# Performance work log

Measured on AMD Instinct MI355X. Metric: run time of the kernel, lower is better.

The kernel has to match this reference:

```python
import jax, jax.numpy as jnp
import numpy as np

POOL = 7          # pool_size
NUM_ROIS = 512    # num_rois
H, W, C = 64, 64, 1024


def setup_inputs() -> dict:
    key = jax.random.key(0)
    k1, k2, k3 = jax.random.split(key, 3)
    img = jax.random.normal(k1, (1, H, W, C), dtype=jnp.float32)
    # rois[0, i] = (x, y, w, h); guarantee x+w <= W and y+h <= H
    xy = jax.random.randint(k2, (1, NUM_ROIS, 2), 0, 32, dtype=jnp.int32)
    wh = jax.random.randint(k3, (1, NUM_ROIS, 2), 8, 33, dtype=jnp.int32)
    rois = jnp.concatenate([xy, wh], axis=-1)
    return {"img": img, "rois": rois}


def _roi_pool_one(img0, roi):
    # img0: [H, W, C]; roi: (x, y, w, h) int32
    # Faithful to tf.image.resize_images(bilinear, align_corners=False, TF1
    # legacy): src = dst * (in_size / out_size), corners clamped to the crop.
    x, y, w, h = roi[0], roi[1], roi[2], roi[3]
    i = jnp.arange(POOL, dtype=jnp.float32)
    sy = i * (h.astype(jnp.float32) / POOL)   # source row within crop
    sx = i * (w.astype(jnp.float32) / POOL)   # source col within crop
    y0 = jnp.floor(sy).astype(jnp.int32)       # always <= h-1 since sy < h
    x0 = jnp.floor(sx).astype(jnp.int32)
    fy = sy - y0.astype(jnp.float32)
    fx = sx - x0.astype(jnp.float32)
    y1 = jnp.minimum(y0 + 1, h - 1)            # clamp to crop edge
    x1 = jnp.minimum(x0 + 1, w - 1)
    gy0, gy1 = y + y0, y + y1                  # global feature-map indices
    gx0, gx1 = x + x0, x + x1
    # gather 4 bilinear corners: each [POOL, POOL, C]
    v00 = img0[gy0[:, None], gx0[None, :]]
    v01 = img0[gy0[:, None], gx1[None, :]]
    v10 = img0[gy1[:, None], gx0[None, :]]
    v11 = img0[gy1[:, None], gx1[None, :]]
    top = v00 + (v01 - v00) * fx[None, :, None]
    bot = v10 + (v11 - v10) * fx[None, :, None]
    return top + (bot - top) * fy[:, None, None]


def reference(img, rois):
    # vmap over ROIs replaces the Python-level per-ROI crop/resize loop
    out = jax.vmap(lambda r: _roi_pool_one(img[0], r))(rois[0])  # [R,P,P,C]
    return out[None]  # [1, num_rois, pool, pool, C]
```

## Files before the change

### kernel.cpp

```cpp
#include <hip/hip_runtime.h>

#define POOL 7
#define NUM_ROIS 512
#define IMG_H 64
#define IMG_W 64
#define IMG_C 1024

__global__ __launch_bounds__(256) void roi_pool_kernel(
    const float* __restrict__ img,
    const int*   __restrict__ rois,
    float*       __restrict__ out)
{
    const int b  = blockIdx.x;
    const int r  = b / 49;
    const int ij = b - r * 49;
    const int i  = ij / 7;
    const int j  = ij - i * 7;

    const int4 roi = reinterpret_cast<const int4*>(rois)[r];
    const int x = roi.x, y = roi.y, w = roi.z, h = roi.w;

    const float sy = (float)i * ((float)h / 7.0f);
    const float sx = (float)j * ((float)w / 7.0f);
    const int y0 = (int)floorf(sy);
    const int x0 = (int)floorf(sx);
    const float fy = sy - (float)y0;
    const float fx = sx - (float)x0;
    const int y1 = min(y0 + 1, h - 1);
    const int x1 = min(x0 + 1, w - 1);
    const int gy0 = y + y0, gy1 = y + y1;
    const int gx0 = x + x0, gx1 = x + x1;

    const int c = threadIdx.x * 4;

    const float4 v00 = *reinterpret_cast<const float4*>(&img[((size_t)gy0 * IMG_W + gx0) * IMG_C + c]);
    const float4 v01 = *reinterpret_cast<const float4*>(&img[((size_t)gy0 * IMG_W + gx1) * IMG_C + c]);
    const float4 v10 = *reinterpret_cast<const float4*>(&img[((size_t)gy1 * IMG_W + gx0) * IMG_C + c]);
    const float4 v11 = *reinterpret_cast<const float4*>(&img[((size_t)gy1 * IMG_W + gx1) * IMG_C + c]);

    float4 res;
    {
        const float t0 = v00.x + (v01.x - v00.x) * fx;
        const float b0 = v10.x + (v11.x - v10.x) * fx;
        res.x = t0 + (b0 - t0) * fy;
    }
    {
        const float t0 = v00.y + (v01.y - v00.y) * fx;
        const float b0 = v10.y + (v11.y - v10.y) * fx;
        res.y = t0 + (b0 - t0) * fy;
    }
    {
        const float t0 = v00.z + (v01.z - v00.z) * fx;
        const float b0 = v10.z + (v11.z - v10.z) * fx;
        res.z = t0 + (b0 - t0) * fy;
    }
    {
        const float t0 = v00.w + (v01.w - v00.w) * fx;
        const float b0 = v10.w + (v11.w - v10.w) * fx;
        res.w = t0 + (b0 - t0) * fy;
    }

    reinterpret_cast<float4*>(out)[(size_t)b * (IMG_C / 4) + threadIdx.x] = res;
}

extern "C" void kernel_launch(void* const* d_in, const int* in_sizes, int n_in,
                              void* d_out, int out_size, void* d_ws, size_t ws_size,
                              hipStream_t stream) {
    const float* img  = (const float*)d_in[0];
    const int*   rois = (const int*)d_in[1];
    float*       out  = (float*)d_out;

    const int grid = NUM_ROIS * POOL * POOL;
    roi_pool_kernel<<<grid, 256, 0, stream>>>(img, rois, out);
}
```

Measured before the change: 143.3 us.

## Process a full pooled row per block with XCD remap and nontemporal stores

```diff
diff --git a/kernel.cpp b/kernel.cpp
--- a/kernel.cpp
+++ b/kernel.cpp
@@ -2,65 +2,67 @@
 
 #define POOL 7
 #define NUM_ROIS 512
-#define IMG_H 64
 #define IMG_W 64
 #define IMG_C 1024
+#define NXCD 8
+
+typedef float vfloat4 __attribute__((ext_vector_type(4)));
 
 __global__ __launch_bounds__(256) void roi_pool_kernel(
     const float* __restrict__ img,
     const int*   __restrict__ rois,
     float*       __restrict__ out)
 {
-    const int b  = blockIdx.x;
-    const int r  = b / 49;
-    const int ij = b - r * 49;
-    const int i  = ij / 7;
-    const int j  = ij - i * 7;
+    const int nwg = NUM_ROIS * POOL;
+    const int cpx = nwg / NXCD;
+    int b = blockIdx.x;
+    b = (b % NXCD) * cpx + b / NXCD;
+
+    const int r = b / POOL;
+    const int i = b - r * POOL;
 
     const int4 roi = reinterpret_cast<const int4*>(rois)[r];
     const int x = roi.x, y = roi.y, w = roi.z, h = roi.w;
 
-    const float sy = (float)i * ((float)h / 7.0f);
-    const float sx = (float)j * ((float)w / 7.0f);
-    const int y0 = (int)floorf(sy);
-    const int x0 = (int)floorf(sx);
+    const float hf = (float)h / 7.0f;
+    const float wf = (float)w / 7.0f;
+    const float sy = (float)i * hf;
+    const int   y0 = (int)floorf(sy);
     const float fy = sy - (float)y0;
-    const float fx = sx - (float)x0;
-    const int y1 = min(y0 + 1, h - 1);
-    const int x1 = min(x0 + 1, w - 1);
-    const int gy0 = y + y0, gy1 = y + y1;
-    const int gx0 = x + x0, gx1 = x + x1;
+    const int   y1 = min(y0 + 1, h - 1);
+
+    const size_t row0 = (size_t)(y + y0) * IMG_W;
+    const size_t row1 = (size_t)(y + y1) * IMG_W;
 
     const int c = threadIdx.x * 4;
 
-    const float4 v00 = *reinterpret_cast<const float4*>(&img[((size_t)gy0 * IMG_W + gx0) * IMG_C + c]);
-    const float4 v01 = *reinterpret_cast<const float4*>(&img[((size_t)gy0 * IMG_W + gx1) * IMG_C + c]);
-    const float4 v10 = *reinterpret_cast<const float4*>(&img[((size_t)gy1 * IMG_W + gx0) * IMG_C + c]);
-    const float4 v11 = *reinterpret_cast<const float4*>(&img[((size_t)gy1 * IMG_W + gx1) * IMG_C + c]);
+    vfloat4 v00[POOL], v01[POOL], v10[POOL], v11[POOL];
+    float   fx[POOL];
 
-    float4 res;
-    {
-        const float t0 = v00.x + (v01.x - v00.x) * fx;
-        const float b0 = v10.x + (v11.x - v10.x) * fx;
-        res.x = t0 + (b0 - t0) * fy;
-    }
-    {
-        const float t0 = v00.y + (v01.y - v00.y) * fx;
-        const float b0 = v10.y + (v11.y - v10.y) * fx;
-        res.y = t0 + (b0 - t0) * fy;
-    }
-    {
-        const float t0 = v00.z + (v01.z - v00.z) * fx;
-        const float b0 = v10.z + (v11.z - v10.z) * fx;
-        res.z = t0 + (b0 - t0) * fy;
-    }
-    {
-        const float t0 = v00.w + (v01.w - v00.w) * fx;
-        const float b0 = v10.w + (v11.w - v10.w) * fx;
-        res.w = t0 + (b0 - t0) * fy;
+#pragma unroll
+    for (int j = 0; j < POOL; ++j) {
+        const float sx = (float)j * wf;
+        const int   x0 = (int)floorf(sx);
+        fx[j] = sx - (float)x0;
+        const int   x1 = min(x0 + 1, w - 1);
+        const int gx0 = x + x0, gx1 = x + x1;
+        v00[j] = *reinterpret_cast<const vfloat4*>(&img[(row0 + gx0) * IMG_C + c]);
+        v01[j] = *reinterpret_cast<const vfloat4*>(&img[(row0 + gx1) * IMG_C + c]);
+        v10[j] = *reinterpret_cast<const vfloat4*>(&img[(row1 + gx0) * IMG_C + c]);
+        v11[j] = *reinterpret_cast<const vfloat4*>(&img[(row1 + gx1) * IMG_C + c]);
     }
 
-    reinterpret_cast<float4*>(out)[(size_t)b * (IMG_C / 4) + threadIdx.x] = res;
+    vfloat4* outv = reinterpret_cast<vfloat4*>(out)
+                  + ((size_t)b * POOL) * (IMG_C / 4) + threadIdx.x;
+
+#pragma unroll
+    for (int j = 0; j < POOL; ++j) {
+        const vfloat4 a = v00[j], bv = v01[j], cv = v10[j], d = v11[j];
+        const vfloat4 t = a + (bv - a) * fx[j];
+        const vfloat4 u = cv + (d - cv) * fx[j];
+        const vfloat4 res = t + (u - t) * fy;
+        __builtin_nontemporal_store(res, &outv[(size_t)j * (IMG_C / 4)]);
+    }
 }
 
 extern "C" void kernel_launch(void* const* d_in, const int* in_sizes, int n_in,
@@ -70,6 +72,6 @@
     const int*   rois = (const int*)d_in[1];
     float*       out  = (float*)d_out;
 
-    const int grid = NUM_ROIS * POOL * POOL;
+    const int grid = NUM_ROIS * POOL;
     roi_pool_kernel<<<grid, 256, 0, stream>>>(img, rois, out);
 }
```

Measured after the change: 143.1 us. No clear change (-0.1%).
